# Optimization experiments

Measured on AMD Instinct MI355X. Metric: run time of the kernel, lower is better.

## Reference

```python
import jax, jax.numpy as jnp
import numpy as np

# frontier sizes per layer (input -> output) and edges per block
N = [400000, 120000, 20000, 4000]
E = [1800000, 200000, 20000]
IN_FEATS, N_HIDDEN, N_CLASSES = 128, 256, 47


def setup_inputs() -> dict:
    key = jax.random.key(0)
    ks = jax.random.split(key, 16)
    inp = {}
    inp["x"] = jax.random.normal(ks[0], (N[0], IN_FEATS), dtype=jnp.float32)
    # block edge lists: src in [0, N[l]), dst in [0, N[l+1))
    for l in range(3):
        inp[f"src{l}"] = jax.random.randint(ks[1 + 2 * l], (E[l],), 0, N[l], dtype=jnp.int32)
        inp[f"dst{l}"] = jax.random.randint(ks[2 + 2 * l], (E[l],), 0, N[l + 1], dtype=jnp.int32)
    dims = [(IN_FEATS, N_HIDDEN), (N_HIDDEN, N_HIDDEN), (N_HIDDEN, N_CLASSES)]
    for l, (din, dout) in enumerate(dims):
        scale = 1.0 / np.sqrt(din)
        inp[f"Ws{l}"] = jax.random.normal(ks[7 + 3 * l], (din, dout), dtype=jnp.float32) * scale
        inp[f"Wn{l}"] = jax.random.normal(ks[8 + 3 * l], (din, dout), dtype=jnp.float32) * scale
        inp[f"b{l}"] = jnp.zeros((dout,), dtype=jnp.float32)
    return inp


def sage_layer(h, src, dst, n_dst, Ws, Wn, b):
    # mean aggregation over incoming edges (gather -> segment-reduce)
    msgs = h[src]  # [E, din]
    neigh_sum = jax.ops.segment_sum(msgs, dst, num_segments=n_dst)
    deg = jax.ops.segment_sum(jnp.ones((dst.shape[0], 1), h.dtype), dst, num_segments=n_dst)
    neigh_mean = neigh_sum / jnp.maximum(deg, 1.0)
    # DGL block convention: dst nodes are the first n_dst src nodes
    return h[:n_dst] @ Ws + neigh_mean @ Wn + b


def reference(x, src0, dst0, src1, dst1, src2, dst2,
              Ws0, Wn0, b0, Ws1, Wn1, b1, Ws2, Wn2, b2):
    h = jax.nn.relu(sage_layer(x, src0, dst0, N[1], Ws0, Wn0, b0))
    h = jax.nn.relu(sage_layer(h, src1, dst1, N[2], Ws1, Wn1, b1))
    h = sage_layer(h, src2, dst2, N[3], Ws2, Wn2, b2)
    return h
```

## Files before the change

### kernel.cpp

```cpp
#include <hip/hip_runtime.h>
#include <hip/hip_bf16.h>

typedef __hip_bfloat16 bf16;
typedef __attribute__((ext_vector_type(8))) short short8;
typedef __attribute__((ext_vector_type(4))) float float4v;

#define N1 120000
#define N2 20000
#define N3 4000
#define E0 1800000
#define E1 200000
#define E2 20000
#define D_IN 128
#define D_HID 256
#define D_OUT 47

__device__ __forceinline__ void stv(float* p, float v) { *p = v; }
__device__ __forceinline__ void stv(bf16* p, float v) { *p = __float2bfloat16(v); }

__device__ __forceinline__ unsigned short f2bu(float v) {
    union { bf16 h; unsigned short u; } c;
    c.h = __float2bfloat16(v);
    return c.u;
}
__device__ __forceinline__ short f2bs(float v) { return (short)f2bu(v); }
__device__ __forceinline__ float bu2f(unsigned short u) { return __uint_as_float(((unsigned)u) << 16); }

__device__ __forceinline__ short8 load8(const bf16* p) {
    union { uint4 u; short8 s; } r;
    r.u = *(const uint4*)p;
    return r.s;
}
__device__ __forceinline__ short8 load8(const float* p) {
    float4 a = *(const float4*)p;
    float4 b = *(const float4*)(p + 4);
    short8 s;
    s[0] = f2bs(a.x); s[1] = f2bs(a.y); s[2] = f2bs(a.z); s[3] = f2bs(a.w);
    s[4] = f2bs(b.x); s[5] = f2bs(b.y); s[6] = f2bs(b.z); s[7] = f2bs(b.w);
    return s;
}

__global__ __launch_bounds__(256) void convert_x(const float* __restrict__ x,
                                                 bf16* __restrict__ xb, int n8) {
    int i = blockIdx.x * blockDim.x + threadIdx.x;
    if (i >= n8) return;
    const float* p = x + (size_t)i * 8;
    float4 a = *(const float4*)p;
    float4 b = *(const float4*)(p + 4);
    union { uint4 u; short s[8]; } o;
    o.s[0] = f2bs(a.x); o.s[1] = f2bs(a.y); o.s[2] = f2bs(a.z); o.s[3] = f2bs(a.w);
    o.s[4] = f2bs(b.x); o.s[5] = f2bs(b.y); o.s[6] = f2bs(b.z); o.s[7] = f2bs(b.w);
    *(uint4*)(xb + (size_t)i * 8) = o.u;
}

__global__ void wt_batch(const float* W0s, const float* W0n, const float* W1s,
                         const float* W1n, const float* W2s, const float* W2n,
                         bf16* T0s, bf16* T0n, bf16* T1s, bf16* T1n, bf16* T2s, bf16* T2n) {
    int i = blockIdx.x * blockDim.x + threadIdx.x;
    const float* W; bf16* T; int K, N, j;
    if      (i <  32768) { W = W0s; T = T0s; K = 128; N = 256; j = i; }
    else if (i <  65536) { W = W0n; T = T0n; K = 128; N = 256; j = i - 32768; }
    else if (i < 131072) { W = W1s; T = T1s; K = 256; N = 256; j = i - 65536; }
    else if (i < 196608) { W = W1n; T = T1n; K = 256; N = 256; j = i - 131072; }
    else if (i < 208896) { W = W2s; T = T2s; K = 256; N = 47;  j = i - 196608; }
    else if (i < 221184) { W = W2n; T = T2n; K = 256; N = 47;  j = i - 208896; }
    else return;
    int n = j / K, k = j - n * K;
    float v = (n < N) ? W[(size_t)k * N + n] : 0.f;
    T[j] = __float2bfloat16(v);
}

__global__ void hist_rank_batch(const int* __restrict__ d0, const int* __restrict__ d1,
                                const int* __restrict__ d2, int* __restrict__ c0,
                                int* __restrict__ c1, int* __restrict__ c2,
                                int* __restrict__ rk0, int* __restrict__ rk1,
                                int* __restrict__ rk2) {
    int i = blockIdx.x * blockDim.x + threadIdx.x;
    if (i < E0) {
        rk0[i] = atomicAdd(&c0[d0[i]], 1);
    } else if (i < E0 + E1) {
        int e = i - E0;
        rk1[e] = atomicAdd(&c1[d1[e]], 1);
    } else if (i < E0 + E1 + E2) {
        int e = i - E0 - E1;
        rk2[e] = atomicAdd(&c2[d2[e]], 1);
    }
}

__global__ void hist_batch(const int* __restrict__ d0, const int* __restrict__ d1,
                           const int* __restrict__ d2, int* __restrict__ c0,
                           int* __restrict__ c1, int* __restrict__ c2) {
    int i = blockIdx.x * blockDim.x + threadIdx.x;
    if (i < E0) atomicAdd(&c0[d0[i]], 1);
    else if (i < E0 + E1) atomicAdd(&c1[d1[i - E0]], 1);
    else if (i < E0 + E1 + E2) atomicAdd(&c2[d2[i - E0 - E1]], 1);
}

__global__ __launch_bounds__(256) void scan_chunk_batch(
    const int* __restrict__ c0, const int* __restrict__ c1, const int* __restrict__ c2,
    int* __restrict__ r0, int* __restrict__ r1, int* __restrict__ r2, int* __restrict__ bsum) {
    __shared__ int sd[256];
    int b = blockIdx.x, t = threadIdx.x;
    const int* cnt; int* out; int* bs; int n, cb;
    if (b < 118)      { cnt = c0; out = r0; bs = bsum;       n = N1; cb = b; }
    else if (b < 138) { cnt = c1; out = r1; bs = bsum + 128; n = N2; cb = b - 118; }
    else              { cnt = c2; out = r2; bs = bsum + 256; n = N3; cb = b - 138; }
    int base = cb * 1024 + t * 4;
    int v[4]; int s = 0;
    #pragma unroll
    for (int j = 0; j < 4; j++) { int i = base + j; v[j] = (i < n) ? cnt[i] : 0; s += v[j]; }
    sd[t] = s;
    __syncthreads();
    for (int off = 1; off < 256; off <<= 1) {
        int x = (t >= off) ? sd[t - off] : 0;
        __syncthreads();
        sd[t] += x;
        __syncthreads();
    }
    int run = sd[t] - s;
    #pragma unroll
    for (int j = 0; j < 4; j++) { int i = base + j; if (i < n) out[i] = run; run += v[j]; }
    if (t == 255) bs[cb] = sd[255];
}

__global__ __launch_bounds__(256) void scan_bsum_batch(int* __restrict__ bsum,
        int* __restrict__ r0, int* __restrict__ r1, int* __restrict__ r2) {
    __shared__ int sd[256];
    int l = blockIdx.x, t = threadIdx.x;
    int B = (l == 0) ? 118 : (l == 1 ? 20 : 4);
    int* bs = bsum + l * 128;
    int s = (t < B) ? bs[t] : 0;
    sd[t] = s;
    __syncthreads();
    for (int off = 1; off < 256; off <<= 1) {
        int x = (t >= off) ? sd[t - off] : 0;
        __syncthreads();
        sd[t] += x;
        __syncthreads();
    }
    if (t < B) bs[t] = sd[t] - s;
    if (t == 255) {
        if (l == 0) r0[N1] = sd[255];
        else if (l == 1) r1[N2] = sd[255];
        else r2[N3] = sd[255];
    }
}

__global__ void scan_add_batch(int* __restrict__ r0, int* __restrict__ r1,
                               int* __restrict__ r2, const int* __restrict__ bsum) {
    int i = blockIdx.x * blockDim.x + threadIdx.x;
    if (i < N1) r0[i] += bsum[i >> 10];
    else if (i < N1 + N2) { int j = i - N1; r1[j] += bsum[128 + (j >> 10)]; }
    else if (i < N1 + N2 + N3) { int j = i - N1 - N2; r2[j] += bsum[256 + (j >> 10)]; }
}

__global__ void csr_fill_rank(const int* __restrict__ s0, const int* __restrict__ d0,
                              const int* __restrict__ s1, const int* __restrict__ d1,
                              const int* __restrict__ s2, const int* __restrict__ d2,
                              const int* __restrict__ rk0, const int* __restrict__ rk1,
                              const int* __restrict__ rk2,
                              const int* __restrict__ r0, const int* __restrict__ r1,
                              const int* __restrict__ r2, int* __restrict__ col0,
                              int* __restrict__ col1, int* __restrict__ col2) {
    int i = blockIdx.x * blockDim.x + threadIdx.x;
    if (i < E0) {
        col0[r0[d0[i]] + rk0[i]] = s0[i];
    } else if (i < E0 + E1) {
        int e = i - E0;
        col1[r1[d1[e]] + rk1[e]] = s1[e];
    } else if (i < E0 + E1 + E2) {
        int e = i - E0 - E1;
        col2[r2[d2[e]] + rk2[e]] = s2[e];
    }
}

__global__ void csr_fill_batch(const int* __restrict__ s0, const int* __restrict__ d0,
                               const int* __restrict__ s1, const int* __restrict__ d1,
                               const int* __restrict__ s2, const int* __restrict__ d2,
                               int* __restrict__ c0, int* __restrict__ c1, int* __restrict__ c2,
                               const int* __restrict__ r0, const int* __restrict__ r1,
                               const int* __restrict__ r2, int* __restrict__ col0,
                               int* __restrict__ col1, int* __restrict__ col2) {
    int i = blockIdx.x * blockDim.x + threadIdx.x;
    if (i < E0) {
        int d = d0[i];
        col0[r0[d] + atomicSub(&c0[d], 1) - 1] = s0[i];
    } else if (i < E0 + E1) {
        int e = i - E0; int d = d1[e];
        col1[r1[d] + atomicSub(&c1[d], 1) - 1] = s1[e];
    } else if (i < E0 + E1 + E2) {
        int e = i - E0 - E1; int d = d2[e];
        col2[r2[d] + atomicSub(&c2[d], 1) - 1] = s2[e];
    }
}

template <int DIN, typename T>
__global__ __launch_bounds__(256) void gather_mean(const T* __restrict__ h,
        const int* __restrict__ rp, const int* __restrict__ col,
        int n_dst, bf16* __restrict__ agg) {
    int gw = (blockIdx.x * blockDim.x + threadIdx.x) >> 6;
    int lane = threadIdx.x & 63;
    if (gw >= n_dst) return;
    int beg = rp[gw], end = rp[gw + 1];
    constexpr int VP = DIN / 64;
    float s[VP] = {};

    auto accum = [&](int srcn) {
        const T* hp = h + (size_t)srcn * DIN + lane * VP;
        if constexpr (sizeof(T) == 4) {
            float2 v = *(const float2*)hp;
            s[0] += v.x; s[1] += v.y;
        } else if constexpr (VP == 2) {
            union { unsigned u; unsigned short us[2]; } r;
            r.u = *(const unsigned*)hp;
            s[0] += bu2f(r.us[0]); s[1] += bu2f(r.us[1]);
        } else {
            union { uint2 u; unsigned short us[4]; } r;
            r.u = *(const uint2*)hp;
            #pragma unroll
            for (int j = 0; j < 4; j++) s[j] += bu2f(r.us[j]);
        }
    };

    int e = beg;
    for (; e + 3 < end; e += 4) {
        int a0 = col[e], a1 = col[e + 1], a2 = col[e + 2], a3 = col[e + 3];
        accum(a0); accum(a1); accum(a2); accum(a3);
    }
    for (; e < end; ++e) accum(col[e]);

    float inv = 1.f / fmaxf((float)(end - beg), 1.f);
    #pragma unroll
    for (int j = 0; j < VP; j++) s[j] *= inv;

    bf16* ap = agg + (size_t)gw * DIN + lane * VP;
    if constexpr (VP == 2) {
        ushort2 o; o.x = f2bu(s[0]); o.y = f2bu(s[1]);
        *(ushort2*)ap = o;
    } else {
        ushort4 o; o.x = f2bu(s[0]); o.y = f2bu(s[1]); o.z = f2bu(s[2]); o.w = f2bu(s[3]);
        *(ushort4*)ap = o;
    }
}

template <int DIN>
__global__ __launch_bounds__(256) void gather_mean_w(const bf16* __restrict__ h,
        const int* __restrict__ rp, const int* __restrict__ col,
        int n_dst, bf16* __restrict__ agg) {
    constexpr int G = DIN / 8;
    constexpr int R = 64 / G;
    int gw = (blockIdx.x * blockDim.x + threadIdx.x) >> 6;
    int lane = threadIdx.x & 63;
    if (gw >= n_dst) return;
    int beg = rp[gw], end = rp[gw + 1];
    int g = lane / G;
    int p = lane & (G - 1);

    float s[8] = {};

    auto accum = [&](const short8& v) {
        #pragma unroll
        for (int j = 0; j < 8; j++) s[j] += bu2f((unsigned short)v[j]);
    };

    int e = beg;
    for (; e + 2 * R <= end; e += 2 * R) {
        int sa = col[e + g];
        int sb = col[e + R + g];
        short8 va = load8(h + (size_t)sa * DIN + p * 8);
        short8 vb = load8(h + (size_t)sb * DIN + p * 8);
        accum(va); accum(vb);
    }
    for (; e + R <= end; e += R) {
        int sa = col[e + g];
        short8 va = load8(h + (size_t)sa * DIN + p * 8);
        accum(va);
    }
    if (e < end) {
        bool act = (e + g) < end;
        int sa = col[act ? (e + g) : beg];
        short8 va = load8(h + (size_t)sa * DIN + p * 8);
        if (act) accum(va);
    }

    #pragma unroll
    for (int m = G; m < 64; m <<= 1) {
        #pragma unroll
        for (int j = 0; j < 8; j++) s[j] += __shfl_xor(s[j], m, 64);
    }

    float inv = 1.f / fmaxf((float)(end - beg), 1.f);
    if (g == 0) {
        union { uint4 u; unsigned short us[8]; } o;
        #pragma unroll
        for (int j = 0; j < 8; j++) o.us[j] = f2bu(s[j] * inv);
        *(uint4*)(agg + (size_t)gw * DIN + p * 8) = o.u;
    }
}

template <typename TA, typename TC, bool RELU>
__global__ __launch_bounds__(256) void gemm_mfma(
    const TA* __restrict__ A, const bf16* __restrict__ Mn,
    const bf16* __restrict__ Wst, const bf16* __restrict__ Wnt,
    const float* __restrict__ bias, TC* __restrict__ C,
    int M, int Nstore, int Npad, int K) {
    __shared__ short As[128][48];
    __shared__ short Bs[128][48];

    int tid = threadIdx.x;
    int m0 = blockIdx.x * 128;
    int n0 = blockIdx.y * 128;
    int lane = tid & 63, wid = tid >> 6;
    int wm = (wid & 1) * 64, wn = (wid >> 1) * 64;
    int l15 = lane & 15, quad = lane >> 4;

    float4v acc[4][4] = {};

    int nsteps = (2 * K) >> 5;
    int r = tid >> 2, c = (tid & 3) << 3;
    for (int s = 0; s < nsteps; ++s) {
        int ks = s << 5;
        bool self = ks < K;
        int ko = self ? ks : ks - K;
        #pragma unroll
        for (int it = 0; it < 2; ++it) {
            int rr = r + it * 64;
            {
                int gm = m0 + rr;
                short8 v = (short8)0;
                if (gm < M) {
                    if (self) v = load8(A  + (size_t)gm * K + ko + c);
                    else      v = load8(Mn + (size_t)gm * K + ko + c);
                }
                *(short8*)&As[rr][c] = v;
            }
            {
                int gn = n0 + rr;
                short8 w = (short8)0;
                if (gn < Npad) {
                    const bf16* Wp = self ? Wst : Wnt;
                    w = load8(Wp + (size_t)gn * K + ko + c);
                }
                *(short8*)&Bs[rr][c] = w;
            }
        }
        __syncthreads();
        short8 af[4], bfr[4];
        #pragma unroll
        for (int i = 0; i < 4; ++i)
            af[i] = *(const short8*)&As[wm + i * 16 + l15][quad * 8];
        #pragma unroll
        for (int j = 0; j < 4; ++j)
            bfr[j] = *(const short8*)&Bs[wn + j * 16 + l15][quad * 8];
        #pragma unroll
        for (int i = 0; i < 4; ++i)
            #pragma unroll
            for (int j = 0; j < 4; ++j)
                acc[i][j] = __builtin_amdgcn_mfma_f32_16x16x32_bf16(af[i], bfr[j], acc[i][j], 0, 0, 0);
        __syncthreads();
    }

    #pragma unroll
    for (int i = 0; i < 4; ++i) {
        #pragma unroll
        for (int j = 0; j < 4; ++j) {
            int gn = n0 + wn + j * 16 + l15;
            if (gn >= Nstore) continue;
            float bv = bias[gn];
            #pragma unroll
            for (int rr = 0; rr < 4; ++rr) {
                int gm = m0 + wm + i * 16 + quad * 4 + rr;
                if (gm >= M) continue;
                float v = acc[i][j][rr] + bv;
                if (RELU) v = fmaxf(v, 0.f);
                stv(&C[(size_t)gm * Nstore + gn], v);
            }
        }
    }
}

extern "C" void kernel_launch(void* const* d_in, const int* in_sizes, int n_in,
                              void* d_out, int out_size, void* d_ws, size_t ws_size,
                              hipStream_t stream) {
    const float* x    = (const float*)d_in[0];
    const int*  src0 = (const int*)d_in[1];
    const int*  dst0 = (const int*)d_in[2];
    const int*  src1 = (const int*)d_in[3];
    const int*  dst1 = (const int*)d_in[4];
    const int*  src2 = (const int*)d_in[5];
    const int*  dst2 = (const int*)d_in[6];
    const float* Ws0 = (const float*)d_in[7];
    const float* Wn0 = (const float*)d_in[8];
    const float* b0  = (const float*)d_in[9];
    const float* Ws1 = (const float*)d_in[10];
    const float* Wn1 = (const float*)d_in[11];
    const float* b1  = (const float*)d_in[12];
    const float* Ws2 = (const float*)d_in[13];
    const float* Wn2 = (const float*)d_in[14];
    const float* b2  = (const float*)d_in[15];
    float* out = (float*)d_out;

    char* W = (char*)d_ws;
    int* cnt0  = (int*)(W + 0);
    int* cnt1  = (int*)(W + 480000);
    int* cnt2  = (int*)(W + 560000);
    int* rp0   = (int*)(W + 576000);
    int* rp1   = (int*)(W + 1056004);
    int* rp2   = (int*)(W + 1136008);
    int* col0  = (int*)(W + 1152016);
    int* col1  = (int*)(W + 8352016);
    int* col2  = (int*)(W + 9152016);
    int* bsum  = (int*)(W + 9232016);
    bf16* Wst0 = (bf16*)(W + 9233552);
    bf16* Wnt0 = (bf16*)(W + 9299088);
    bf16* Wst1 = (bf16*)(W + 9364624);
    bf16* Wnt1 = (bf16*)(W + 9495696);
    bf16* Wst2 = (bf16*)(W + 9626768);
    bf16* Wnt2 = (bf16*)(W + 9651344);

    const size_t BASE = 9676032;
    const bool use_xb = ws_size >= (size_t)205000000;
    bf16* xb = (bf16*)(W + BASE);
    size_t agg0_off = BASE + (use_xb ? 102400000 : 0);
    bf16* agg0 = (bf16*)(W + agg0_off);
    bf16* h1   = (bf16*)(W + agg0_off + 30720000);
    bf16* agg1 = (bf16*)(W + BASE);
    bf16* h2   = (bf16*)(W + BASE + 10240000);
    bf16* agg2 = (bf16*)(W + BASE + 20480000);

    const bool ranked = ws_size >= (size_t)219000000;
    int* rk0 = (int*)(W + 210000000);
    int* rk1 = (int*)(W + 217200000);
    int* rk2 = (int*)(W + 218000000);

    hipMemsetAsync(W, 0, 576000, stream);
    if (use_xb) {
        int n8 = 400000 * D_IN / 8;
        convert_x<<<(n8 + 255) / 256, 256, 0, stream>>>(x, xb, n8);
    }
    wt_batch<<<(221184 + 255) / 256, 256, 0, stream>>>(Ws0, Wn0, Ws1, Wn1, Ws2, Wn2,
                                                       Wst0, Wnt0, Wst1, Wnt1, Wst2, Wnt2);
    const int ETOT = E0 + E1 + E2;
    if (ranked) {
        hist_rank_batch<<<(ETOT + 255) / 256, 256, 0, stream>>>(dst0, dst1, dst2,
                                                                cnt0, cnt1, cnt2,
                                                                rk0, rk1, rk2);
    } else {
        hist_batch<<<(ETOT + 255) / 256, 256, 0, stream>>>(dst0, dst1, dst2, cnt0, cnt1, cnt2);
    }
    scan_chunk_batch<<<142, 256, 0, stream>>>(cnt0, cnt1, cnt2, rp0, rp1, rp2, bsum);
    scan_bsum_batch<<<3, 256, 0, stream>>>(bsum, rp0, rp1, rp2);
    scan_add_batch<<<(N1 + N2 + N3 + 255) / 256, 256, 0, stream>>>(rp0, rp1, rp2, bsum);
    if (ranked) {
        csr_fill_rank<<<(ETOT + 255) / 256, 256, 0, stream>>>(src0, dst0, src1, dst1, src2, dst2,
                                                              rk0, rk1, rk2, rp0, rp1, rp2,
                                                              col0, col1, col2);
    } else {
        csr_fill_batch<<<(ETOT + 255) / 256, 256, 0, stream>>>(src0, dst0, src1, dst1, src2, dst2,
                                                               cnt0, cnt1, cnt2, rp0, rp1, rp2,
                                                               col0, col1, col2);
    }

    if (use_xb) {
        gather_mean_w<D_IN><<<(N1 + 3) / 4, 256, 0, stream>>>(xb, rp0, col0, N1, agg0);
        dim3 grid((N1 + 127) / 128, 2);
        gemm_mfma<bf16, bf16, true><<<grid, 256, 0, stream>>>(xb, agg0, Wst0, Wnt0, b0, h1, N1, 256, 256, 128);
    } else {
        gather_mean<D_IN, float><<<(N1 + 3) / 4, 256, 0, stream>>>(x, rp0, col0, N1, agg0);
        dim3 grid((N1 + 127) / 128, 2);
        gemm_mfma<float, bf16, true><<<grid, 256, 0, stream>>>(x, agg0, Wst0, Wnt0, b0, h1, N1, 256, 256, 128);
    }

    gather_mean_w<D_HID><<<(N2 + 3) / 4, 256, 0, stream>>>(h1, rp1, col1, N2, agg1);
    {
        dim3 grid((N2 + 127) / 128, 2);
        gemm_mfma<bf16, bf16, true><<<grid, 256, 0, stream>>>(h1, agg1, Wst1, Wnt1, b1, h2, N2, 256, 256, 256);
    }

    gather_mean_w<D_HID><<<(N3 + 3) / 4, 256, 0, stream>>>(h2, rp2, col2, N3, agg2);
    {
        dim3 grid((N3 + 127) / 128, 1);
        gemm_mfma<bf16, float, false><<<grid, 256, 0, stream>>>(h2, agg2, Wst2, Wnt2, b2, out, N3, 47, 48, 256);
    }
}
```

Before: 682.5 us.

## Add direct-to-LDS MFMA GEMM, shrink rank arrays to u16, repack workspace

Adds a new bf16 GEMM kernel that streams A and weight tiles straight into LDS with global_load_lds and runs 16x16x32 bf16 MFMAs. It is used for all three layers when the workspace is large enough. The per-edge rank arrays are narrowed from int to unsigned short, halving their write and read traffic in the CSR build. The layer-2 weights are padded to 128 rows so the new kernel can load full tiles without bounds checks. The workspace layout is rearranged to fit. The new GEMM is single-buffered with two barriers per 32-wide K step, so load latency is not overlapped with compute. The u16 ranks assume no destination has more than 65535 incoming edges.

New measurement: 702.7 us. 1.03x slower.

```diff
diff --git a/kernel.cpp b/kernel.cpp
--- a/kernel.cpp
+++ b/kernel.cpp
@@ -40,6 +40,13 @@
     return s;
 }
 
+__device__ __forceinline__ void llds16(const void* g, void* l) {
+    __builtin_amdgcn_global_load_lds(
+        (const __attribute__((address_space(1))) void*)g,
+        (__attribute__((address_space(3))) void*)l,
+        16, 0, 0);
+}
+
 __global__ __launch_bounds__(256) void convert_x(const float* __restrict__ x,
                                                  bf16* __restrict__ xb, int n8) {
     int i = blockIdx.x * blockDim.x + threadIdx.x;
@@ -62,8 +69,8 @@
     else if (i <  65536) { W = W0n; T = T0n; K = 128; N = 256; j = i - 32768; }
     else if (i < 131072) { W = W1s; T = T1s; K = 256; N = 256; j = i - 65536; }
     else if (i < 196608) { W = W1n; T = T1n; K = 256; N = 256; j = i - 131072; }
-    else if (i < 208896) { W = W2s; T = T2s; K = 256; N = 47;  j = i - 196608; }
-    else if (i < 221184) { W = W2n; T = T2n; K = 256; N = 47;  j = i - 208896; }
+    else if (i < 229376) { W = W2s; T = T2s; K = 256; N = 47;  j = i - 196608; }
+    else if (i < 262144) { W = W2n; T = T2n; K = 256; N = 47;  j = i - 229376; }
     else return;
     int n = j / K, k = j - n * K;
     float v = (n < N) ? W[(size_t)k * N + n] : 0.f;
@@ -73,17 +80,18 @@
 __global__ void hist_rank_batch(const int* __restrict__ d0, const int* __restrict__ d1,
                                 const int* __restrict__ d2, int* __restrict__ c0,
                                 int* __restrict__ c1, int* __restrict__ c2,
-                                int* __restrict__ rk0, int* __restrict__ rk1,
-                                int* __restrict__ rk2) {
+                                unsigned short* __restrict__ rk0,
+                                unsigned short* __restrict__ rk1,
+                                unsigned short* __restrict__ rk2) {
     int i = blockIdx.x * blockDim.x + threadIdx.x;
     if (i < E0) {
-        rk0[i] = atomicAdd(&c0[d0[i]], 1);
+        rk0[i] = (unsigned short)atomicAdd(&c0[d0[i]], 1);
     } else if (i < E0 + E1) {
         int e = i - E0;
-        rk1[e] = atomicAdd(&c1[d1[e]], 1);
+        rk1[e] = (unsigned short)atomicAdd(&c1[d1[e]], 1);
     } else if (i < E0 + E1 + E2) {
         int e = i - E0 - E1;
-        rk2[e] = atomicAdd(&c2[d2[e]], 1);
+        rk2[e] = (unsigned short)atomicAdd(&c2[d2[e]], 1);
     }
 }
 
@@ -157,20 +165,21 @@
 __global__ void csr_fill_rank(const int* __restrict__ s0, const int* __restrict__ d0,
                               const int* __restrict__ s1, const int* __restrict__ d1,
                               const int* __restrict__ s2, const int* __restrict__ d2,
-                              const int* __restrict__ rk0, const int* __restrict__ rk1,
-                              const int* __restrict__ rk2,
+                              const unsigned short* __restrict__ rk0,
+                              const unsigned short* __restrict__ rk1,
+                              const unsigned short* __restrict__ rk2,
                               const int* __restrict__ r0, const int* __restrict__ r1,
                               const int* __restrict__ r2, int* __restrict__ col0,
                               int* __restrict__ col1, int* __restrict__ col2) {
     int i = blockIdx.x * blockDim.x + threadIdx.x;
     if (i < E0) {
-        col0[r0[d0[i]] + rk0[i]] = s0[i];
+        col0[r0[d0[i]] + (int)rk0[i]] = s0[i];
     } else if (i < E0 + E1) {
         int e = i - E0;
-        col1[r1[d1[e]] + rk1[e]] = s1[e];
+        col1[r1[d1[e]] + (int)rk1[e]] = s1[e];
     } else if (i < E0 + E1 + E2) {
         int e = i - E0 - E1;
-        col2[r2[d2[e]] + rk2[e]] = s2[e];
+        col2[r2[d2[e]] + (int)rk2[e]] = s2[e];
     }
 }
 
@@ -295,6 +304,74 @@
         #pragma unroll
         for (int j = 0; j < 8; j++) o.us[j] = f2bu(s[j] * inv);
         *(uint4*)(agg + (size_t)gw * DIN + p * 8) = o.u;
+    }
+}
+
+template <typename TC, bool RELU>
+__global__ __launch_bounds__(256) void gemm_dl(
+    const bf16* __restrict__ A, const bf16* __restrict__ Mn,
+    const bf16* __restrict__ Wst, const bf16* __restrict__ Wnt,
+    const float* __restrict__ bias, TC* __restrict__ C,
+    int M, int Nstore, int K) {
+    __shared__ short As[128][32];
+    __shared__ short Bs[128][32];
+
+    int tid = threadIdx.x;
+    int m0 = blockIdx.x * 128;
+    int n0 = blockIdx.y * 128;
+    int lane = tid & 63, wid = tid >> 6;
+    int wm = (wid & 1) * 64, wn = (wid >> 1) * 64;
+    int l15 = lane & 15, quad = lane >> 4;
+    int sr = lane >> 2;
+    int sc = (lane & 3) << 3;
+
+    float4v acc[4][4] = {};
+
+    int nsteps = (2 * K) >> 5;
+    for (int s = 0; s < nsteps; ++s) {
+        int ks = s << 5;
+        bool self = ks < K;
+        int ko = (self ? ks : ks - K) + sc;
+        const bf16* Ab = self ? A : Mn;
+        const bf16* Bb = self ? Wst : Wnt;
+        #pragma unroll
+        for (int it = 0; it < 2; ++it) {
+            int rbase = wid * 32 + it * 16;
+            llds16(Ab + (size_t)(m0 + rbase + sr) * K + ko, &As[rbase][0]);
+            llds16(Bb + (size_t)(n0 + rbase + sr) * K + ko, &Bs[rbase][0]);
+        }
+        __syncthreads();
+        short8 af[4], bfr[4];
+        #pragma unroll
+        for (int i = 0; i < 4; ++i)
+            af[i] = *(const short8*)&As[wm + i * 16 + l15][quad * 8];
+        #pragma unroll
+        for (int j = 0; j < 4; ++j)
+            bfr[j] = *(const short8*)&Bs[wn + j * 16 + l15][quad * 8];
+        #pragma unroll
+        for (int i = 0; i < 4; ++i)
+            #pragma unroll
+            for (int j = 0; j < 4; ++j)
+                acc[i][j] = __builtin_amdgcn_mfma_f32_16x16x32_bf16(af[i], bfr[j], acc[i][j], 0, 0, 0);
+        __syncthreads();
+    }
+
+    #pragma unroll
+    for (int i = 0; i < 4; ++i) {
+        #pragma unroll
+        for (int j = 0; j < 4; ++j) {
+            int gn = n0 + wn + j * 16 + l15;
+            if (gn >= Nstore) continue;
+            float bv = bias[gn];
+            #pragma unroll
+            for (int rr = 0; rr < 4; ++rr) {
+                int gm = m0 + wm + i * 16 + quad * 4 + rr;
+                if (gm >= M) continue;
+                float v = acc[i][j][rr] + bv;
+                if (RELU) v = fmaxf(v, 0.f);
+                stv(&C[(size_t)gm * Nstore + gn], v);
+            }
+        }
     }
 }
 
@@ -416,32 +493,30 @@
     bf16* Wst1 = (bf16*)(W + 9364624);
     bf16* Wnt1 = (bf16*)(W + 9495696);
     bf16* Wst2 = (bf16*)(W + 9626768);
-    bf16* Wnt2 = (bf16*)(W + 9651344);
-
-    const size_t BASE = 9676032;
-    const bool use_xb = ws_size >= (size_t)205000000;
-    bf16* xb = (bf16*)(W + BASE);
-    size_t agg0_off = BASE + (use_xb ? 102400000 : 0);
-    bf16* agg0 = (bf16*)(W + agg0_off);
-    bf16* h1   = (bf16*)(W + agg0_off + 30720000);
+    bf16* Wnt2 = (bf16*)(W + 9692304);
+
+    const size_t BASE = 9757840;
+    const bool big = ws_size >= (size_t)209000000;
+    bf16* xb   = (bf16*)(W + BASE);
+    size_t o   = BASE + (big ? 102400000 : 0);
+    bf16* agg0 = (bf16*)(W + o);
+    bf16* h1   = (bf16*)(W + o + 30736384);
     bf16* agg1 = (bf16*)(W + BASE);
-    bf16* h2   = (bf16*)(W + BASE + 10240000);
-    bf16* agg2 = (bf16*)(W + BASE + 20480000);
-
-    const bool ranked = ws_size >= (size_t)219000000;
-    int* rk0 = (int*)(W + 210000000);
-    int* rk1 = (int*)(W + 217200000);
-    int* rk2 = (int*)(W + 218000000);
+    bf16* h2   = (bf16*)(W + BASE + 10289152);
+    bf16* agg2 = (bf16*)(W + BASE + 20529152);
+    unsigned short* rk0 = (unsigned short*)(W + o + 30736384 + 61440000);
+    unsigned short* rk1 = (unsigned short*)((char*)rk0 + 3600000);
+    unsigned short* rk2 = (unsigned short*)((char*)rk1 + 400000);
 
     hipMemsetAsync(W, 0, 576000, stream);
-    if (use_xb) {
+    if (big) {
         int n8 = 400000 * D_IN / 8;
         convert_x<<<(n8 + 255) / 256, 256, 0, stream>>>(x, xb, n8);
     }
-    wt_batch<<<(221184 + 255) / 256, 256, 0, stream>>>(Ws0, Wn0, Ws1, Wn1, Ws2, Wn2,
-                                                       Wst0, Wnt0, Wst1, Wnt1, Wst2, Wnt2);
+    wt_batch<<<262144 / 256, 256, 0, stream>>>(Ws0, Wn0, Ws1, Wn1, Ws2, Wn2,
+                                               Wst0, Wnt0, Wst1, Wnt1, Wst2, Wnt2);
     const int ETOT = E0 + E1 + E2;
-    if (ranked) {
+    if (big) {
         hist_rank_batch<<<(ETOT + 255) / 256, 256, 0, stream>>>(dst0, dst1, dst2,
                                                                 cnt0, cnt1, cnt2,
                                                                 rk0, rk1, rk2);
@@ -451,7 +526,7 @@
     scan_chunk_batch<<<142, 256, 0, stream>>>(cnt0, cnt1, cnt2, rp0, rp1, rp2, bsum);
     scan_bsum_batch<<<3, 256, 0, stream>>>(bsum, rp0, rp1, rp2);
     scan_add_batch<<<(N1 + N2 + N3 + 255) / 256, 256, 0, stream>>>(rp0, rp1, rp2, bsum);
-    if (ranked) {
+    if (big) {
         csr_fill_rank<<<(ETOT + 255) / 256, 256, 0, stream>>>(src0, dst0, src1, dst1, src2, dst2,
                                                               rk0, rk1, rk2, rp0, rp1, rp2,
                                                               col0, col1, col2);
@@ -461,10 +536,10 @@
                                                                col0, col1, col2);
     }
 
-    if (use_xb) {
+    if (big) {
         gather_mean_w<D_IN><<<(N1 + 3) / 4, 256, 0, stream>>>(xb, rp0, col0, N1, agg0);
         dim3 grid((N1 + 127) / 128, 2);
-        gemm_mfma<bf16, bf16, true><<<grid, 256, 0, stream>>>(xb, agg0, Wst0, Wnt0, b0, h1, N1, 256, 256, 128);
+        gemm_dl<bf16, true><<<grid, 256, 0, stream>>>(xb, agg0, Wst0, Wnt0, b0, h1, N1, 256, 128);
     } else {
         gather_mean<D_IN, float><<<(N1 + 3) / 4, 256, 0, stream>>>(x, rp0, col0, N1, agg0);
         dim3 grid((N1 + 127) / 128, 2);
@@ -472,14 +547,20 @@
     }
 
     gather_mean_w<D_HID><<<(N2 + 3) / 4, 256, 0, stream>>>(h1, rp1, col1, N2, agg1);
-    {
+    if (big) {
+        dim3 grid((N2 + 127) / 128, 2);
+        gemm_dl<bf16, true><<<grid, 256, 0, stream>>>(h1, agg1, Wst1, Wnt1, b1, h2, N2, 256, 256);
+    } else {
         dim3 grid((N2 + 127) / 128, 2);
         gemm_mfma<bf16, bf16, true><<<grid, 256, 0, stream>>>(h1, agg1, Wst1, Wnt1, b1, h2, N2, 256, 256, 256);
     }
 
     gather_mean_w<D_HID><<<(N3 + 3) / 4, 256, 0, stream>>>(h2, rp2, col2, N3, agg2);
-    {
+    if (big) {
         dim3 grid((N3 + 127) / 128, 1);
-        gemm_mfma<bf16, float, false><<<grid, 256, 0, stream>>>(h2, agg2, Wst2, Wnt2, b2, out, N3, 47, 48, 256);
-    }
-}
+        gemm_dl<float, false><<<grid, 256, 0, stream>>>(h2, agg2, Wst2, Wnt2, b2, out, N3, 47, 256);
+    } else {
+        dim3 grid((N3 + 127) / 128, 1);
+        gemm_mfma<bf16, float, false><<<grid, 256, 0, stream>>>(h2, agg2, Wst2, Wnt2, b2, out, N3, 47, 128, 256);
+    }
+}
```
